# Kernel tuning notes

Measured on AMD Instinct MI355X. Metric: run time of the kernel, lower is better.

The kernel has to match this reference:

```python
import jax, jax.numpy as jnp
import numpy as np

N = 8192      # nodes
K_NN = 32     # kNN neighbors (module default k=32)
E = N * 16    # edges for TAGConv graph
EPS = 1e-5    # BatchNorm eps


def setup_inputs() -> dict:
    key = jax.random.key(0)
    ks = iter(jax.random.split(key, 64))
    def lin(i, o):
        return jax.random.normal(next(ks), (i, o), jnp.float32) / np.float32(np.sqrt(i))
    def vec(c, scale=0.02):
        return jax.random.normal(next(ks), (c,), jnp.float32) * scale
    inp = {}
    inp["pos"] = jax.random.normal(next(ks), (N, 3), jnp.float32)
    inp["x"] = jax.random.normal(next(ks), (N, 4), jnp.float32)
    inp["edge_index"] = jax.random.randint(next(ks), (2, E), 0, N, jnp.int32)
    # conv1 edge-MLP [2*3, 64, 64, 64]
    inp["mlp1_W1"] = lin(6, 64)
    inp["mlp1_W23"] = jnp.stack([lin(64, 64), lin(64, 64)])
    inp["mlp1_b"] = jnp.stack([vec(64) for _ in range(3)])
    inp["mlp1_g"] = 1.0 + jnp.stack([vec(64) for _ in range(3)])
    inp["mlp1_beta"] = jnp.stack([vec(64) for _ in range(3)])
    # conv2 edge-MLP [2*64, 128]
    inp["mlp2_W"] = lin(128, 128); inp["mlp2_b"] = vec(128)
    inp["mlp2_g"] = 1.0 + vec(128); inp["mlp2_beta"] = vec(128)
    # lin1 MLP [128+64, 512]
    inp["lin1_W"] = lin(192, 512); inp["lin1_b"] = vec(512)
    inp["lin1_g"] = 1.0 + vec(512); inp["lin1_beta"] = vec(512)
    # TAGConv(4,64,K=3) and TAGConv(64,128,K=3): K+1 hop weights each, shared bias
    inp["tag1_W"] = jnp.stack([lin(4, 64) for _ in range(4)]); inp["tag1_b"] = vec(64)
    inp["tag2_W"] = jnp.stack([lin(64, 128) for _ in range(4)]); inp["tag2_b"] = vec(128)
    # lin_gcnn1 MLP [128+64, 512]
    inp["lin2_W"] = lin(192, 512); inp["lin2_b"] = vec(512)
    inp["lin2_g"] = 1.0 + vec(512); inp["lin2_beta"] = vec(512)
    # mix_output: MLP[1024,512] -> Dropout -> MLP[512,256] -> Dropout -> Lin(256,1)
    inp["mix1_W"] = lin(1024, 512); inp["mix1_b"] = vec(512)
    inp["mix1_g"] = 1.0 + vec(512); inp["mix1_beta"] = vec(512)
    inp["mix2_W"] = lin(512, 256); inp["mix2_b"] = vec(256)
    inp["mix2_g"] = 1.0 + vec(256); inp["mix2_beta"] = vec(256)
    inp["out_W"] = lin(256, 1); inp["out_b"] = vec(1)
    return inp


def _bn_relu_lin(h, W, b, g, beta):
    # Seq(Linear, ReLU, BatchNorm1d) with training-mode (batch) statistics
    h = jax.nn.relu(h @ W + b)
    mu = jnp.mean(h, axis=0)
    var = jnp.var(h, axis=0)
    return g * (h - mu) * jax.lax.rsqrt(var + EPS) + beta


def _knn_idx(x, k):
    # brute-force kNN (loop=False: self excluded); indices are non-differentiable
    x = jax.lax.stop_gradient(x)
    sq = jnp.sum(x * x, axis=1)
    d = sq[:, None] + sq[None, :] - 2.0 * (x @ x.T)   # [N,N] squared dists
    n = x.shape[0]
    d = d.at[jnp.arange(n), jnp.arange(n)].set(jnp.inf)
    _, idx = jax.lax.top_k(-d, k)
    return idx                                        # [N,k]


def _edge_conv(x, k, mlp_fn):
    # DynamicEdgeConv: kNN graph on x, message MLP([x_i, x_j - x_i]), max-aggregate
    idx = _knn_idx(x, k)
    xj = x[idx]                                       # [N,k,C]
    xi = jnp.broadcast_to(x[:, None, :], xj.shape)
    e = jnp.concatenate([xi, xj - xi], axis=-1).reshape(-1, 2 * x.shape[1])
    h = mlp_fn(e)                                     # [N*k, C_out]
    return jnp.max(h.reshape(x.shape[0], k, -1), axis=1)


def _tag_conv(x, W, b, row, col, norm):
    # TAGConv: out = sum_{m=0..K} (D^-1/2 A D^-1/2)^m x @ W_m + b
    out = x @ W[0]
    h = x
    for m in range(1, W.shape[0]):
        h = jax.ops.segment_sum(norm[:, None] * h[row], col, num_segments=x.shape[0])
        out = out + h @ W[m]
    return out + b


def reference(pos, x, edge_index, mlp1_W1, mlp1_W23, mlp1_b, mlp1_g, mlp1_beta,
              mlp2_W, mlp2_b, mlp2_g, mlp2_beta, lin1_W, lin1_b, lin1_g, lin1_beta,
              tag1_W, tag1_b, tag2_W, tag2_b, lin2_W, lin2_b, lin2_g, lin2_beta,
              mix1_W, mix1_b, mix1_g, mix1_beta, mix2_W, mix2_b, mix2_g, mix2_beta,
              out_W, out_b):
    def mlp1(e):
        h = _bn_relu_lin(e, mlp1_W1, mlp1_b[0], mlp1_g[0], mlp1_beta[0])
        h = _bn_relu_lin(h, mlp1_W23[0], mlp1_b[1], mlp1_g[1], mlp1_beta[1])
        return _bn_relu_lin(h, mlp1_W23[1], mlp1_b[2], mlp1_g[2], mlp1_beta[2])
    def mlp2(e):
        return _bn_relu_lin(e, mlp2_W, mlp2_b, mlp2_g, mlp2_beta)

    # --- DGCNN branch on positions ---
    x1 = _edge_conv(pos, K_NN, mlp1)                  # [N,64]
    x2 = _edge_conv(x1, K_NN, mlp2)                   # [N,128]
    out_dg = _bn_relu_lin(jnp.concatenate([x1, x2], axis=1),
                          lin1_W, lin1_b, lin1_g, lin1_beta)  # [N,512]

    # --- TAGConv branch on node features ---
    row, col = edge_index[0], edge_index[1]
    deg = jax.ops.segment_sum(jnp.ones(row.shape[0], x.dtype), col, num_segments=x.shape[0])
    dinv = jnp.where(deg > 0, jax.lax.rsqrt(jnp.maximum(deg, 1.0)), 0.0)
    norm = dinv[row] * dinv[col]
    g1 = jax.nn.relu(_tag_conv(x, tag1_W, tag1_b, row, col, norm))    # [N,64]
    g2 = jax.nn.relu(_tag_conv(g1, tag2_W, tag2_b, row, col, norm))   # [N,128]
    out_g = _bn_relu_lin(jnp.concatenate([g1, g2], axis=1),
                         lin2_W, lin2_b, lin2_g, lin2_beta)           # [N,512]

    # --- mix head (dropout = identity in eval) ---
    h = jnp.concatenate([out_dg, out_g], axis=1)      # [N,1024]
    h = _bn_relu_lin(h, mix1_W, mix1_b, mix1_g, mix1_beta)
    h = _bn_relu_lin(h, mix2_W, mix2_b, mix2_g, mix2_beta)
    return h @ out_W + out_b                          # [N,1]
```

## Files before the change

kernel.cpp:

```cpp
#include <hip/hip_runtime.h>
#include <cstdint>
#include <cstddef>

#define BN_EPS 1e-5f
#define K1CAP 1024
#define K2CAP 640

typedef short short8 __attribute__((ext_vector_type(8)));
typedef float f32x4 __attribute__((ext_vector_type(4)));
typedef unsigned long long ull;

__device__ __forceinline__ unsigned int ordf(float d) {
  unsigned int u = __float_as_uint(d);
  return (u >> 31) ? ~u : (u | 0x80000000u);
}
__device__ __forceinline__ unsigned short f2bf(float f) {
  unsigned u = __float_as_uint(f);
  u += 0x7fffu + ((u >> 16) & 1u);
  return (unsigned short)(u >> 16);
}
__device__ __forceinline__ float bf2f(unsigned short h) {
  return __uint_as_float(((unsigned)h) << 16);
}

#define BPAD 72

__global__ __launch_bounds__(256)
void mk_gemm_mfma(const float* __restrict__ A,
                  const short* __restrict__ A8h, const short* __restrict__ A8l,
                  const float* __restrict__ src, const int* __restrict__ gidx, int srcC,
                  const float* __restrict__ bnA,
                  const short* __restrict__ Wh, const short* __restrict__ Wl,
                  int ldk, int koff, int lda,
                  const float* __restrict__ bias,
                  float* __restrict__ C, int ldc,
                  int M, int N, int K, int flags,
                  float* __restrict__ statsP,
                  float* __restrict__ mxp, float* __restrict__ mnp) {
  __shared__ short Ah[64][BPAD], Al[64][BPAD], Bh[64][BPAD], Bl[64][BPAD];
  __shared__ float ssum[64], ssq[64];
  int tid = threadIdx.x, lane = tid & 63, wid = tid >> 6;
  int wr = wid >> 1, wc = wid & 1;
  int r0 = blockIdx.x * 64, n0 = blockIdx.y * 64;
  int sr = tid >> 2, sc = (tid & 3) * 16;
  f32x4 zero4 = {0.f, 0.f, 0.f, 0.f};
  f32x4 acc[2][2] = {{zero4, zero4}, {zero4, zero4}};
  short8 rAh[2], rAl[2], rBh[2], rBl[2];

  auto stage = [&](int kt) {
    const short* bh = &Wh[(size_t)(n0 + sr) * ldk + koff + kt + sc];
    const short* bl = &Wl[(size_t)(n0 + sr) * ldk + koff + kt + sc];
    rBh[0] = *(const short8*)bh; rBh[1] = *(const short8*)(bh + 8);
    rBl[0] = *(const short8*)bl; rBl[1] = *(const short8*)(bl + 8);
    if (A8h) {
      const short* ah = &A8h[(size_t)(r0 + sr) * lda + kt + sc];
      const short* al = &A8l[(size_t)(r0 + sr) * lda + kt + sc];
      rAh[0] = *(const short8*)ah; rAh[1] = *(const short8*)(ah + 8);
      rAl[0] = *(const short8*)al; rAl[1] = *(const short8*)(al + 8);
    } else {
      float v[16];
      if (flags & 32) {
        int gr = r0 + sr;
        int i = gr >> 5; int j = gidx[gr];
        const float* pi = &A[(size_t)i * srcC + kt + sc];
        const float* pj = &src[(size_t)j * srcC + kt + sc];
        float va[16], vb[16];
        *(float4*)&va[0]  = *(const float4*)&pi[0];
        *(float4*)&va[4]  = *(const float4*)&pi[4];
        *(float4*)&va[8]  = *(const float4*)&pi[8];
        *(float4*)&va[12] = *(const float4*)&pi[12];
        *(float4*)&vb[0]  = *(const float4*)&pj[0];
        *(float4*)&vb[4]  = *(const float4*)&pj[4];
        *(float4*)&vb[8]  = *(const float4*)&pj[8];
        *(float4*)&vb[12] = *(const float4*)&pj[12];
#pragma unroll
        for (int e = 0; e < 16; ++e) v[e] = fmaxf(va[e] + vb[e], 0.f);
      } else {
        const float* ap = &A[(size_t)(r0 + sr) * lda + kt + sc];
        *(float4*)&v[0]  = *(const float4*)&ap[0];
        *(float4*)&v[4]  = *(const float4*)&ap[4];
        *(float4*)&v[8]  = *(const float4*)&ap[8];
        *(float4*)&v[12] = *(const float4*)&ap[12];
      }
      if (bnA) {
#pragma unroll
        for (int e = 0; e < 16; ++e) {
          int gk = kt + sc + e;
          v[e] = fmaf(bnA[gk], v[e], bnA[1024 + gk]);
        }
      }
#pragma unroll
      for (int e = 0; e < 16; ++e) {
        unsigned short h = f2bf(v[e]);
        rAh[e >> 3][e & 7] = (short)h;
        rAl[e >> 3][e & 7] = (short)f2bf(v[e] - bf2f(h));
      }
    }
  };

  stage(0);
  for (int kt = 0; kt < K; kt += 64) {
    *(short8*)&Ah[sr][sc]     = rAh[0];
    *(short8*)&Ah[sr][sc + 8] = rAh[1];
    *(short8*)&Al[sr][sc]     = rAl[0];
    *(short8*)&Al[sr][sc + 8] = rAl[1];
    *(short8*)&Bh[sr][sc]     = rBh[0];
    *(short8*)&Bh[sr][sc + 8] = rBh[1];
    *(short8*)&Bl[sr][sc]     = rBl[0];
    *(short8*)&Bl[sr][sc + 8] = rBl[1];
    __syncthreads();
    if (kt + 64 < K) stage(kt + 64);
    int ar = wr * 32 + (lane & 15);
    int br = wc * 32 + (lane & 15);
#pragma unroll
    for (int kk = 0; kk < 2; ++kk) {
      int kof = kk * 32 + (lane >> 4) * 8;
      short8 a_h[2], a_l[2], b_h[2], b_l[2];
#pragma unroll
      for (int t = 0; t < 2; ++t) {
        a_h[t] = *(const short8*)&Ah[ar + t * 16][kof];
        a_l[t] = *(const short8*)&Al[ar + t * 16][kof];
        b_h[t] = *(const short8*)&Bh[br + t * 16][kof];
        b_l[t] = *(const short8*)&Bl[br + t * 16][kof];
      }
#pragma unroll
      for (int mt = 0; mt < 2; ++mt)
#pragma unroll
        for (int nt = 0; nt < 2; ++nt) {
          acc[mt][nt] = __builtin_amdgcn_mfma_f32_16x16x32_bf16(a_h[mt], b_h[nt], acc[mt][nt], 0, 0, 0);
          acc[mt][nt] = __builtin_amdgcn_mfma_f32_16x16x32_bf16(a_h[mt], b_l[nt], acc[mt][nt], 0, 0, 0);
          acc[mt][nt] = __builtin_amdgcn_mfma_f32_16x16x32_bf16(a_l[mt], b_h[nt], acc[mt][nt], 0, 0, 0);
        }
    }
    __syncthreads();
  }
  bool dostat = (flags & 8) != 0, domx = (flags & 16) != 0;
  float lsum[2] = {0.f, 0.f}, lsq[2] = {0.f, 0.f};
  float lmx[2] = {-3.4e38f, -3.4e38f}, lmn[2] = {3.4e38f, 3.4e38f};
#pragma unroll
  for (int nt = 0; nt < 2; ++nt) {
    int gc = n0 + wc * 32 + nt * 16 + (lane & 15);
#pragma unroll
    for (int mt = 0; mt < 2; ++mt)
#pragma unroll
      for (int i = 0; i < 4; ++i) {
        int gr = r0 + wr * 32 + mt * 16 + (lane >> 4) * 4 + i;
        float v = acc[mt][nt][i];
        if (bias) v += bias[gc];
        if (flags & 1) v += C[(size_t)gr * ldc + gc];
        if (flags & 2) v = fmaxf(v, 0.f);
        if (!domx) C[(size_t)gr * ldc + gc] = v;
        lsum[nt] += v; lsq[nt] = fmaf(v, v, lsq[nt]);
        lmx[nt] = fmaxf(lmx[nt], v); lmn[nt] = fminf(lmn[nt], v);
      }
  }
  if (dostat || domx) {
#pragma unroll
    for (int nt = 0; nt < 2; ++nt) {
#pragma unroll
      for (int m = 16; m <= 32; m <<= 1) {
        lsum[nt] += __shfl_xor(lsum[nt], m, 64);
        lsq[nt] += __shfl_xor(lsq[nt], m, 64);
        lmx[nt] = fmaxf(lmx[nt], __shfl_xor(lmx[nt], m, 64));
        lmn[nt] = fminf(lmn[nt], __shfl_xor(lmn[nt], m, 64));
      }
    }
    if (domx && lane < 16) {
      int node = blockIdx.x * 2 + wr;
#pragma unroll
      for (int nt = 0; nt < 2; ++nt) {
        int gc = n0 + wc * 32 + nt * 16 + lane;
        mxp[(size_t)node * N + gc] = lmx[nt];
        mnp[(size_t)node * N + gc] = lmn[nt];
      }
    }
    if (dostat) {
      if (tid < 64) { ssum[tid] = 0.f; ssq[tid] = 0.f; }
      __syncthreads();
      if (lane < 16) {
#pragma unroll
        for (int nt = 0; nt < 2; ++nt) {
          int ct = wc * 32 + nt * 16 + lane;
          atomicAdd(&ssum[ct], lsum[nt]);
          atomicAdd(&ssq[ct], lsq[nt]);
        }
      }
      __syncthreads();
      if (tid < 64) {
        int slot = blockIdx.x & 63;
        int gc = n0 + tid;
        atomicAdd(&statsP[(size_t)slot * 1024 + gc], ssum[tid]);
        atomicAdd(&statsP[(size_t)slot * 1024 + 512 + gc], ssq[tid]);
      }
    }
  }
}

__global__ void mk_wcvt(const float* __restrict__ W, short* __restrict__ Wh,
                        short* __restrict__ Wl, int K, int N) {
  int g = blockIdx.x * 256 + threadIdx.x;
  if (g >= K * N) return;
  int k = g / N, n = g - k * N;
  float v = W[g];
  unsigned short h = f2bf(v);
  Wh[(size_t)n * K + k] = (short)h;
  Wl[(size_t)n * K + k] = (short)f2bf(v - bf2f(h));
}
__global__ void mk_wcvt2(const float* __restrict__ W, short* __restrict__ Dh,
                         short* __restrict__ Dl, short* __restrict__ Vh,
                         short* __restrict__ Vl) {
  int g = blockIdx.x * 256 + threadIdx.x;
  if (g >= 64 * 128) return;
  int k = g >> 7, n = g & 127;
  float u = W[k * 128 + n], vv = W[(64 + k) * 128 + n];
  float d = u - vv;
  unsigned short h = f2bf(d);
  Dh[n * 64 + k] = (short)h; Dl[n * 64 + k] = (short)f2bf(d - bf2f(h));
  h = f2bf(vv);
  Vh[n * 64 + k] = (short)h; Vl[n * 64 + k] = (short)f2bf(vv - bf2f(h));
}

__global__ void mk_conv1nodes(const float* __restrict__ pos, const float* __restrict__ W1,
                              const float* __restrict__ b1, float* __restrict__ Pp,
                              float* __restrict__ Qn) {
  int g = blockIdx.x * 256 + threadIdx.x;
  if (g >= 8192 * 64) return;
  int i = g >> 6, c = g & 63;
  float p0 = pos[i * 3], p1 = pos[i * 3 + 1], p2 = pos[i * 3 + 2];
  float q = p0 * W1[192 + c] + p1 * W1[256 + c] + p2 * W1[320 + c];
  Qn[g] = q;
  Pp[g] = p0 * W1[c] + p1 * W1[64 + c] + p2 * W1[128 + c] - q + b1[c];
}

__global__ __launch_bounds__(256)
void mk_stats1(const float* __restrict__ Pp, const float* __restrict__ Qn,
               const int* __restrict__ idx1, float* __restrict__ statsP) {
  __shared__ int sidx[512];
  int tid = threadIdx.x;
  int c = tid & 63, grp = tid >> 6;
  int nb = blockIdx.x * 16;
  if (tid < 256) {
    sidx[tid] = idx1[nb * 32 + tid];
    sidx[tid + 256] = idx1[nb * 32 + 256 + tid];
  }
  __syncthreads();
  float s = 0.f, q = 0.f;
  for (int ln = 0; ln < 16; ++ln) {
    float pv = Pp[(size_t)(nb + ln) * 64 + c];
    for (int e = grp; e < 32; e += 4) {
      int j = sidx[ln * 32 + e];
      float v = fmaxf(pv + Qn[(size_t)j * 64 + c], 0.f);
      s += v; q = fmaf(v, v, q);
    }
  }
  int slot = (blockIdx.x * 4 + grp) & 63;
  atomicAdd(&statsP[(size_t)slot * 1024 + c], s);
  atomicAdd(&statsP[(size_t)slot * 1024 + 512 + c], q);
}

__global__ __launch_bounds__(128)
void mk_econv2(const float* __restrict__ R, const float* __restrict__ T,
               const int* __restrict__ st_i, float* __restrict__ mxp,
               float* __restrict__ mnp, float* __restrict__ statsP) {
  __shared__ int sidx[256];
  int tid = threadIdx.x;
  int nb = blockIdx.x * 8;
  sidx[tid] = st_i[nb * 32 + tid];
  sidx[tid + 128] = st_i[nb * 32 + 128 + tid];
  __syncthreads();
  float s = 0.f, q = 0.f;
  for (int ln = 0; ln < 8; ++ln) {
    int i = nb + ln;
    float rv = R[(size_t)i * 128 + tid];
    float mx = -3.4e38f, mn = 3.4e38f;
    for (int e = 0; e < 32; ++e) {
      int j = sidx[ln * 32 + e];
      float v = fmaxf(rv + T[(size_t)j * 128 + tid], 0.f);
      mx = fmaxf(mx, v); mn = fminf(mn, v);
      s += v; q = fmaf(v, v, q);
    }
    mxp[(size_t)i * 128 + tid] = mx;
    mnp[(size_t)i * 128 + tid] = mn;
  }
  int slot = blockIdx.x & 63;
  atomicAdd(&statsP[(size_t)slot * 1024 + tid], s);
  atomicAdd(&statsP[(size_t)slot * 1024 + 512 + tid], q);
}

__global__ void mk_bnfinS(const float* __restrict__ sb, const float* __restrict__ g,
                          const float* __restrict__ beta, float* __restrict__ bno,
                          float Minv, int Cdim) {
  int c = blockIdx.x * 256 + threadIdx.x;
  if (c >= Cdim) return;
  float s = 0.f, q = 0.f;
  for (int sl = 0; sl < 64; ++sl) {
    s += sb[(size_t)sl * 1024 + c];
    q += sb[(size_t)sl * 1024 + 512 + c];
  }
  float mu = s * Minv;
  float var = q * Minv - mu * mu;
  float a = g[c] * rsqrtf(var + BN_EPS);
  bno[c] = a;
  bno[1024 + c] = beta[c] - a * mu;
}

__global__ void mk_finx1(const float* __restrict__ mx, const float* __restrict__ mn,
                         const float* __restrict__ bn, float* __restrict__ xc,
                         short* __restrict__ x1h, short* __restrict__ x1l) {
  int g = blockIdx.x * 256 + threadIdx.x;
  if (g >= 8192 * 64) return;
  int i = g >> 6, c = g & 63;
  float a = bn[c], b = bn[1024 + c];
  float v = (a > 0.f) ? fmaf(a, mx[g], b) : fmaf(a, mn[g], b);
  xc[(size_t)i * 192 + c] = v;
  unsigned short h = f2bf(v);
  x1h[g] = (short)h;
  x1l[g] = (short)f2bf(v - bf2f(h));
}
__global__ void mk_finx2(const float* __restrict__ mx, const float* __restrict__ mn,
                         const float* __restrict__ bn, float* __restrict__ xcB) {
  int g = blockIdx.x * 256 + threadIdx.x;
  if (g >= 8192 * 128) return;
  int i = g >> 7, c = g & 127;
  float a = bn[c], b = bn[1024 + c];
  xcB[(size_t)i * 192 + c] = (a > 0.f) ? fmaf(a, mx[g], b) : fmaf(a, mn[g], b);
}

__global__ void mk_posq(const float* __restrict__ pos, float4* __restrict__ posq) {
  int i = blockIdx.x * 256 + threadIdx.x;
  if (i >= 8192) return;
  float x = pos[i * 3], y = pos[i * 3 + 1], z = pos[i * 3 + 2];
  float s = fmaf(z, z, fmaf(y, y, x * x));
  posq[i] = make_float4(x, y, z, s);
}

__device__ __forceinline__ unsigned wave_kth8(unsigned v) {
  unsigned T = 0;
#pragma unroll
  for (int b = 31; b >= 0; --b) {
    unsigned cand = T | (1u << b);
    int c = __popcll(__ballot(v < cand));
    if (c < 8) T = cand;
  }
  return T;
}

__global__ __launch_bounds__(256)
void mk_knn1(const float4* __restrict__ posq, int* __restrict__ idxout) {
  __shared__ ull buf[K1CAP];
  __shared__ unsigned Tw[4];
  __shared__ unsigned cnt;
  int q = blockIdx.x, tid = threadIdx.x;
  int lane = tid & 63, wid = tid >> 6;
  float4 pq = posq[q];
  if (tid == 0) cnt = 0;
  unsigned key[32];
  unsigned vmin = 0xFFFFFFFFu;
#pragma unroll
  for (int c = 0; c < 32; ++c) {
    int j = c * 256 + tid;
    float4 pj = posq[j];
    float d = pq.w + pj.w - 2.f * (pq.x * pj.x + pq.y * pj.y + pq.z * pj.z);
    unsigned k = (j == q) ? 0xFFFFFFFFu : ordf(d);
    key[c] = k;
    vmin = vmin < k ? vmin : k;
  }
  unsigned T = wave_kth8(vmin);
  if (lane == 0) Tw[wid] = T;
  __syncthreads();
  unsigned Tmax = max(max(Tw[0], Tw[1]), max(Tw[2], Tw[3]));
#pragma unroll
  for (int c = 0; c < 32; ++c) {
    if (key[c] <= Tmax) {
      int j = c * 256 + tid;
      unsigned s = atomicAdd(&cnt, 1u);
      if (s < K1CAP) buf[s] = (((ull)key[c]) << 32) | (unsigned)j;
    }
  }
  __syncthreads();
  int m = cnt < (unsigned)K1CAP ? (int)cnt : K1CAP;
  for (int e = tid; e < m; e += 256) {
    ull mine = buf[e];
    int rank = 0;
    for (int f = 0; f < m; ++f) rank += (buf[f] < mine) ? 1 : 0;
    if (rank < 32) idxout[q * 32 + rank] = (int)(unsigned)(mine & 0xFFFFFFFFu);
  }
}

__global__ __launch_bounds__(256)
void mk_knn2(const float* __restrict__ S, const float* __restrict__ sq,
             int c0, int first,
             unsigned* __restrict__ st_k, int* __restrict__ st_i) {
  __shared__ ull buf[K2CAP];
  __shared__ unsigned Tw[4];
  __shared__ unsigned cnt;
  int q = blockIdx.x, tid = threadIdx.x;
  int lane = tid & 63, wid = tid >> 6;
  float sqq = sq[q];
  if (tid == 0) cnt = 0;
  unsigned key[8];
  unsigned vmin = 0xFFFFFFFFu;
#pragma unroll
  for (int c = 0; c < 8; ++c) {
    int t = c * 256 + tid;
    int j = c0 + t;
    float d = sqq + sq[j] - 2.f * S[(size_t)q * 2048 + t];
    unsigned k = (j == q) ? 0xFFFFFFFFu : ordf(d);
    key[c] = k;
    vmin = vmin < k ? vmin : k;
  }
  unsigned T = wave_kth8(vmin);
  if (lane == 0) Tw[wid] = T;
  __syncthreads();
  unsigned Tmax = max(max(Tw[0], Tw[1]), max(Tw[2], Tw[3]));
#pragma unroll
  for (int c = 0; c < 8; ++c) {
    if (key[c] <= Tmax) {
      int j = c0 + c * 256 + tid;
      unsigned s = atomicAdd(&cnt, 1u);
      if (s < K2CAP) buf[s] = (((ull)key[c]) << 32) | (unsigned)j;
    }
  }
  if (!first && tid < 32) {
    ull k = (((ull)st_k[q * 32 + tid]) << 32) | (unsigned)st_i[q * 32 + tid];
    unsigned s = atomicAdd(&cnt, 1u);
    if (s < K2CAP) buf[s] = k;
  }
  __syncthreads();
  int m = cnt < (unsigned)K2CAP ? (int)cnt : K2CAP;
  for (int e = tid; e < m; e += 256) {
    ull mine = buf[e];
    int rank = 0;
    for (int f = 0; f < m; ++f) rank += (buf[f] < mine) ? 1 : 0;
    if (rank < 32) {
      st_k[q * 32 + rank] = (unsigned)(mine >> 32);
      st_i[q * 32 + rank] = (int)(unsigned)(mine & 0xFFFFFFFFu);
    }
  }
}

#define GBM 64
#define GBN 64
#define GBK 16

__global__ __launch_bounds__(256)
void mk_gemm(const float* __restrict__ A, const float* __restrict__ W, int ldw,
             const float* __restrict__ bias, float* __restrict__ C, int ldc,
             int M, int N, int K, int flags) {
  __shared__ float As[GBK][GBM + 4];
  __shared__ float Ws[GBK][GBN];
  int tid = threadIdx.x;
  int r0 = blockIdx.x * GBM, n0 = blockIdx.y * GBN;
  int ty = tid >> 4, tx = tid & 15;
  float acc[4][4] = {};
  for (int kt = 0; kt < K; kt += GBK) {
#pragma unroll
    for (int it = 0; it < 4; ++it) {
      int l = it * 256 + tid;
      int r = l >> 4, kk = l & 15;
      int gr = r0 + r, gk = kt + kk;
      float v = 0.f;
      if (gk < K && gr < M) v = A[(size_t)gr * K + gk];
      As[kk][r] = v;
      int kw = l >> 6, nw = l & 63;
      int gkw = kt + kw;
      Ws[kw][nw] = (gkw < K && (n0 + nw) < N) ? W[(size_t)gkw * ldw + n0 + nw] : 0.f;
    }
    __syncthreads();
#pragma unroll
    for (int kk = 0; kk < GBK; ++kk) {
      float4 a4 = *(const float4*)&As[kk][ty * 4];
      float4 b4 = *(const float4*)&Ws[kk][tx * 4];
      float av[4] = {a4.x, a4.y, a4.z, a4.w};
      float bv[4] = {b4.x, b4.y, b4.z, b4.w};
#pragma unroll
      for (int i = 0; i < 4; ++i)
#pragma unroll
        for (int j = 0; j < 4; ++j)
          acc[i][j] = fmaf(av[i], bv[j], acc[i][j]);
    }
    __syncthreads();
  }
#pragma unroll
  for (int i = 0; i < 4; ++i) {
    int gr = r0 + ty * 4 + i;
    if (gr >= M) continue;
#pragma unroll
    for (int j = 0; j < 4; ++j) {
      int gc = n0 + tx * 4 + j;
      if (gc >= N) continue;
      float v = acc[i][j];
      if (bias) v += bias[gc];
      if (flags & 1) v += C[(size_t)gr * ldc + gc];
      if (flags & 2) v = fmaxf(v, 0.f);
      C[(size_t)gr * ldc + gc] = v;
    }
  }
}

__global__ void mk_sqnorm(const float* __restrict__ x, int ld, float* __restrict__ sq,
                          int Npts, int Cdim) {
  int i = blockIdx.x * blockDim.x + threadIdx.x;
  if (i >= Npts) return;
  float s = 0.f;
  for (int c = 0; c < Cdim; ++c) { float v = x[(size_t)i * ld + c]; s = fmaf(v, v, s); }
  sq[i] = s;
}

__global__ void mk_count(const int* __restrict__ col, int* __restrict__ cnt, int E) {
  int e = blockIdx.x * 256 + threadIdx.x;
  if (e < E) atomicAdd(&cnt[col[e]], 1);
}
__global__ __launch_bounds__(1024)
void mk_scan(const int* __restrict__ cnt, int* __restrict__ offp,
             int* __restrict__ cur, float* __restrict__ dinvf) {
  __shared__ int wsum[16];
  __shared__ int wexc[16];
  int t = threadIdx.x, lane = t & 63, w = t >> 6;
  int v[8]; int s = 0;
  int base = t * 8;
#pragma unroll
  for (int k = 0; k < 8; ++k) { v[k] = s; s += cnt[base + k]; }
  int sc = s;
#pragma unroll
  for (int off2 = 1; off2 < 64; off2 <<= 1) {
    int n = __shfl_up(sc, off2, 64);
    if (lane >= off2) sc += n;
  }
  if (lane == 63) wsum[w] = sc;
  __syncthreads();
  if (w == 0) {
    int x = (lane < 16) ? wsum[lane] : 0;
    int scx = x;
#pragma unroll
    for (int off2 = 1; off2 < 16; off2 <<= 1) {
      int n = __shfl_up(scx, off2, 64);
      if (lane >= off2) scx += n;
    }
    if (lane < 16) wexc[lane] = scx - x;
  }
  __syncthreads();
  int texc = wexc[w] + (sc - s);
#pragma unroll
  for (int k = 0; k < 8; ++k) {
    int o = texc + v[k];
    offp[base + k] = o;
    cur[base + k] = o;
    int d = cnt[base + k];
    dinvf[base + k] = (d > 0) ? rsqrtf((float)(d < 1 ? 1 : d)) : 0.f;
  }
  if (t == 1023) offp[8192] = texc + s;
}
__global__ void mk_fill(const int* __restrict__ row, const int* __restrict__ col,
                        const float* __restrict__ dinvf, int* __restrict__ cur,
                        int* __restrict__ crow, float* __restrict__ cw, int E) {
  int e = blockIdx.x * 256 + threadIdx.x;
  if (e >= E) return;
  int c = col[e], r = row[e];
  int s = atomicAdd(&cur[c], 1);
  crow[s] = r;
  cw[s] = dinvf[r] * dinvf[c];
}
__global__ void mk_prop64(const float* __restrict__ in, int in_ld,
                          const int* __restrict__ offp, const int* __restrict__ crow,
                          const float* __restrict__ cw, float* __restrict__ out, int out_ld) {
  int gid = blockIdx.x * 256 + threadIdx.x;
  if (gid >= 8192 * 16) return;
  int col = gid >> 4, c4 = (gid & 15) * 4;
  int s0 = offp[col], s1 = offp[col + 1];
  float a0 = 0, a1 = 0, a2 = 0, a3 = 0;
  for (int s = s0; s < s1; ++s) {
    int r = crow[s]; float w = cw[s];
    float4 v = *(const float4*)&in[(size_t)r * in_ld + c4];
    a0 = fmaf(w, v.x, a0); a1 = fmaf(w, v.y, a1);
    a2 = fmaf(w, v.z, a2); a3 = fmaf(w, v.w, a3);
  }
  float4 o = {a0, a1, a2, a3};
  *(float4*)&out[(size_t)col * out_ld + c4] = o;
}
__global__ void mk_prop4(const float* __restrict__ in, int in_ld,
                         const int* __restrict__ offp, const int* __restrict__ crow,
                         const float* __restrict__ cw, float* __restrict__ out, int out_ld) {
  int col = blockIdx.x * 256 + threadIdx.x;
  if (col >= 8192) return;
  int s0 = offp[col], s1 = offp[col + 1];
  float a0 = 0, a1 = 0, a2 = 0, a3 = 0;
  for (int s = s0; s < s1; ++s) {
    int r = crow[s]; float w = cw[s];
    float4 v = *(const float4*)&in[(size_t)r * in_ld];
    a0 = fmaf(w, v.x, a0); a1 = fmaf(w, v.y, a1);
    a2 = fmaf(w, v.z, a2); a3 = fmaf(w, v.w, a3);
  }
  float4 o = {a0, a1, a2, a3};
  *(float4*)&out[(size_t)col * out_ld] = o;
}
__global__ void mk_pack4(const float* __restrict__ xin, float* __restrict__ H1) {
  int g = blockIdx.x * 256 + threadIdx.x;
  if (g >= 8192 * 4) return;
  H1[(size_t)(g >> 2) * 16 + (g & 3)] = xin[g];
}
__global__ void mk_copy64(const float* __restrict__ gcv, float* __restrict__ H2) {
  int g = blockIdx.x * 256 + threadIdx.x;
  if (g >= 8192 * 64) return;
  H2[(size_t)(g >> 6) * 256 + (g & 63)] = gcv[(size_t)(g >> 6) * 192 + (g & 63)];
}

__global__ __launch_bounds__(256)
void mk_gemv_out(const float* __restrict__ h, const float* __restrict__ bn,
                 const float* __restrict__ w, const float* __restrict__ b,
                 float* __restrict__ out, int Npts) {
  int row = blockIdx.x * 4 + (threadIdx.x >> 6);
  int lane = threadIdx.x & 63;
  if (row >= Npts) return;
  int c = lane * 4;
  float4 v = *(const float4*)&h[(size_t)row * 256 + c];
  float s = (bn[c] * v.x + bn[1024 + c]) * w[c]
          + (bn[c + 1] * v.y + bn[1024 + c + 1]) * w[c + 1]
          + (bn[c + 2] * v.z + bn[1024 + c + 2]) * w[c + 2]
          + (bn[c + 3] * v.w + bn[1024 + c + 3]) * w[c + 3];
#pragma unroll
  for (int off = 32; off; off >>= 1) s += __shfl_xor(s, off, 64);
  if (lane == 0) out[row] = s + b[0];
}

extern "C" void kernel_launch(void* const* d_in, const int* in_sizes, int n_in,
                              void* d_out, int out_size, void* d_ws, size_t ws_size,
                              hipStream_t stream) {
  const int N = 8192;
  const int NE = N * 32;
  const float* pos = (const float*)d_in[0];
  const float* xin = (const float*)d_in[1];
  const int* ei = (const int*)d_in[2];
  const int E = in_sizes[2] / 2;
  const int* erow = ei;
  const int* ecol = ei + E;
  const float* mlp1_W1  = (const float*)d_in[3];
  const float* mlp1_W23 = (const float*)d_in[4];
  const float* mlp1_b   = (const float*)d_in[5];
  const float* mlp1_g   = (const float*)d_in[6];
  const float* mlp1_be  = (const float*)d_in[7];
  const float* mlp2_W   = (const float*)d_in[8];
  const float* mlp2_b   = (const float*)d_in[9];
  const float* mlp2_g   = (const float*)d_in[10];
  const float* mlp2_be  = (const float*)d_in[11];
  const float* lin1_W   = (const float*)d_in[12];
  const float* lin1_b   = (const float*)d_in[13];
  const float* lin1_g   = (const float*)d_in[14];
  const float* lin1_be  = (const float*)d_in[15];
  const float* tag1_W   = (const float*)d_in[16];
  const float* tag1_b   = (const float*)d_in[17];
  const float* tag2_W   = (const float*)d_in[18];
  const float* tag2_b   = (const float*)d_in[19];
  const float* lin2_W   = (const float*)d_in[20];
  const float* lin2_b   = (const float*)d_in[21];
  const float* lin2_g   = (const float*)d_in[22];
  const float* lin2_be  = (const float*)d_in[23];
  const float* mix1_W   = (const float*)d_in[24];
  const float* mix1_b   = (const float*)d_in[25];
  const float* mix1_g   = (const float*)d_in[26];
  const float* mix1_be  = (const float*)d_in[27];
  const float* mix2_W   = (const float*)d_in[28];
  const float* mix2_b   = (const float*)d_in[29];
  const float* mix2_g   = (const float*)d_in[30];
  const float* mix2_be  = (const float*)d_in[31];
  const float* outW     = (const float*)d_in[32];
  const float* outB     = (const float*)d_in[33];

  char* base = (char*)d_ws;
  size_t off = 0;
  auto alloc = [&](size_t b) -> void* {
    void* p = base + off;
    off += (b + 255) & ~(size_t)255;
    return p;
  };
  float* BIG = (float*)alloc(134217728ull);
  float* h2    = BIG;
  float* Sb    = BIG;
  float* mhcat = BIG;
  float* mh1   = BIG + 8388608;
  float* mh2   = BIG + 12582912;
  float* H2    = BIG + 16777216;
  int*   idx1 = (int*)alloc((size_t)NE * 4);
  unsigned* st_k = (unsigned*)alloc((size_t)NE * 4);
  int*   st_i = (int*)alloc((size_t)NE * 4);
  float* xc  = (float*)alloc((size_t)N * 192 * 4);
  float* gc  = (float*)alloc((size_t)N * 192 * 4);
  float4* posq = (float4*)alloc((size_t)N * 16);
  float* sqx = (float*)alloc((size_t)N * 4);
  float* Pp  = (float*)alloc((size_t)N * 64 * 4);
  float* Qn  = (float*)alloc((size_t)N * 64 * 4);
  float* Rb  = (float*)alloc((size_t)N * 128 * 4);
  float* Tb  = (float*)alloc((size_t)N * 128 * 4);
  float* mx1 = (float*)alloc((size_t)N * 64 * 4);
  float* mn1 = (float*)alloc((size_t)N * 64 * 4);
  float* mx2 = (float*)alloc((size_t)N * 128 * 4);
  float* mn2 = (float*)alloc((size_t)N * 128 * 4);
  float* H1  = (float*)alloc((size_t)N * 16 * 4);
  float* dinvf = (float*)alloc((size_t)N * 4);
  int* cnt     = (int*)alloc((size_t)N * 4);
  int* csr_off = (int*)alloc((size_t)(N + 1) * 4);
  int* cursor  = (int*)alloc((size_t)N * 4);
  int* csr_row = (int*)alloc((size_t)E * 4);
  float* csr_w = (float*)alloc((size_t)E * 4);
  float* slotAll = (float*)alloc((size_t)8 * 64 * 1024 * 4);
  auto slot = [&](int i) { return slotAll + (size_t)i * 64 * 1024; };
  float* bnb = (float*)alloc(8 * 2048 * 4);
  auto bnp = [&](int i) { return bnb + (size_t)i * 2048; };
  float* bnM = bnp(4);
  auto salloc = [&](size_t n) { return (short*)alloc(n * 2); };
  short* w23a_h = salloc(4096);   short* w23a_l = salloc(4096);
  short* w23b_h = salloc(4096);   short* w23b_l = salloc(4096);
  short* wd2_h  = salloc(8192);   short* wd2_l  = salloc(8192);
  short* wv2_h  = salloc(8192);   short* wv2_l  = salloc(8192);
  short* wl1_h  = salloc(98304);  short* wl1_l  = salloc(98304);
  short* wt2_h  = salloc(32768);  short* wt2_l  = salloc(32768);
  short* wl2_h  = salloc(98304);  short* wl2_l  = salloc(98304);
  short* wx1_h  = salloc(524288); short* wx1_l  = salloc(524288);
  short* wx2_h  = salloc(131072); short* wx2_l  = salloc(131072);
  short* x1h    = salloc(524288); short* x1l    = salloc(524288);

  auto gemmF = [&](const float* A, const short* A8h, const short* A8l,
                   const float* src, const int* gidx, int srcC, const float* bnA,
                   const short* Wh_, const short* Wl_, int ldk, int koff, int lda,
                   const float* bias, float* Cp, int ldc,
                   int M, int Nn, int Kk, int flags,
                   float* stP = nullptr, float* mxP = nullptr, float* mnP = nullptr) {
    dim3 g(M / 64, Nn / 64);
    mk_gemm_mfma<<<g, 256, 0, stream>>>(A, A8h, A8l, src, gidx, srcC, bnA,
                                        Wh_, Wl_, ldk, koff, lda, bias, Cp, ldc,
                                        M, Nn, Kk, flags, stP, mxP, mnP);
  };
  auto wcvt = [&](const float* W, short* Wh_, short* Wl_, int Kk, int Nn) {
    mk_wcvt<<<(Kk * Nn + 255) / 256, 256, 0, stream>>>(W, Wh_, Wl_, Kk, Nn);
  };

  hipMemsetAsync(slotAll, 0, (size_t)8 * 64 * 1024 * 4, stream);
  hipMemsetAsync(cnt, 0, (size_t)N * 4, stream);
  wcvt(mlp1_W23,        w23a_h, w23a_l, 64, 64);
  wcvt(mlp1_W23 + 4096, w23b_h, w23b_l, 64, 64);
  mk_wcvt2<<<(64 * 128 + 255) / 256, 256, 0, stream>>>(mlp2_W, wd2_h, wd2_l, wv2_h, wv2_l);
  wcvt(lin1_W, wl1_h, wl1_l, 192, 512);
  wcvt(tag2_W, wt2_h, wt2_l, 256, 128);
  wcvt(lin2_W, wl2_h, wl2_l, 192, 512);
  wcvt(mix1_W, wx1_h, wx1_l, 1024, 512);
  wcvt(mix2_W, wx2_h, wx2_l, 512, 256);

  mk_posq<<<32, 256, 0, stream>>>(pos, posq);
  mk_knn1<<<N, 256, 0, stream>>>(posq, idx1);

  mk_conv1nodes<<<(N * 64 + 255) / 256, 256, 0, stream>>>(pos, mlp1_W1, mlp1_b, Pp, Qn);
  mk_stats1<<<512, 256, 0, stream>>>(Pp, Qn, idx1, slot(0));
  mk_bnfinS<<<1, 256, 0, stream>>>(slot(0), mlp1_g, mlp1_be, bnp(0), 1.f / NE, 64);
  gemmF(Pp, nullptr, nullptr, Qn, idx1, 64, bnp(0),
        w23a_h, w23a_l, 64, 0, 64, mlp1_b + 64, h2, 64, NE, 64, 64, 2 | 8 | 32, slot(1));
  mk_bnfinS<<<1, 256, 0, stream>>>(slot(1), mlp1_g + 64, mlp1_be + 64, bnp(1), 1.f / NE, 64);
  gemmF(h2, nullptr, nullptr, nullptr, nullptr, 0, bnp(1),
        w23b_h, w23b_l, 64, 0, 64, mlp1_b + 128, nullptr, 64, NE, 64, 64, 2 | 8 | 16,
        slot(2), mx1, mn1);
  mk_bnfinS<<<1, 256, 0, stream>>>(slot(2), mlp1_g + 128, mlp1_be + 128, bnp(2), 1.f / NE, 64);
  mk_finx1<<<(N * 64 + 255) / 256, 256, 0, stream>>>(mx1, mn1, bnp(2), xc, x1h, x1l);

  mk_sqnorm<<<32, 256, 0, stream>>>(xc, 192, sqx, N, 64);
  for (int c = 0; c < 4; ++c) {
    gemmF(nullptr, x1h, x1l, nullptr, nullptr, 0, nullptr,
          x1h + (size_t)c * 2048 * 64, x1l + (size_t)c * 2048 * 64, 64, 0, 64,
          nullptr, Sb, 2048, N, 2048, 64, 0);
    mk_knn2<<<N, 256, 0, stream>>>(Sb, sqx, c * 2048, c == 0 ? 1 : 0, st_k, st_i);
  }

  gemmF(nullptr, x1h, x1l, nullptr, nullptr, 0, nullptr,
        wd2_h, wd2_l, 64, 0, 64, mlp2_b, Rb, 128, N, 128, 64, 0);
  gemmF(nullptr, x1h, x1l, nullptr, nullptr, 0, nullptr,
        wv2_h, wv2_l, 64, 0, 64, nullptr, Tb, 128, N, 128, 64, 0);
  mk_econv2<<<N / 8, 128, 0, stream>>>(Rb, Tb, st_i, mx2, mn2, slot(3));
  mk_bnfinS<<<1, 256, 0, stream>>>(slot(3), mlp2_g, mlp2_be, bnp(3), 1.f / NE, 128);
  mk_finx2<<<(N * 128 + 255) / 256, 256, 0, stream>>>(mx2, mn2, bnp(3), xc + 64);

  gemmF(xc, nullptr, nullptr, nullptr, nullptr, 0, nullptr,
        wl1_h, wl1_l, 192, 0, 192, lin1_b, mhcat, 1024, N, 512, 192, 2 | 8, slot(4));
  mk_bnfinS<<<2, 256, 0, stream>>>(slot(4), lin1_g, lin1_be, bnM, 1.f / N, 512);

  mk_count<<<(E + 255) / 256, 256, 0, stream>>>(ecol, cnt, E);
  mk_scan<<<1, 1024, 0, stream>>>(cnt, csr_off, cursor, dinvf);
  mk_fill<<<(E + 255) / 256, 256, 0, stream>>>(erow, ecol, dinvf, cursor, csr_row, csr_w, E);
  mk_pack4<<<(N * 4 + 255) / 256, 256, 0, stream>>>(xin, H1);
  mk_prop4<<<32, 256, 0, stream>>>(xin, 4, csr_off, csr_row, csr_w, H1 + 4, 16);
  mk_prop4<<<32, 256, 0, stream>>>(H1 + 4, 16, csr_off, csr_row, csr_w, H1 + 8, 16);
  mk_prop4<<<32, 256, 0, stream>>>(H1 + 8, 16, csr_off, csr_row, csr_w, H1 + 12, 16);
  mk_gemm<<<dim3(128, 1), 256, 0, stream>>>(H1, tag1_W, 64, tag1_b, gc, 192, N, 64, 16, 2);
  mk_copy64<<<(N * 64 + 255) / 256, 256, 0, stream>>>(gc, H2);
  mk_prop64<<<512, 256, 0, stream>>>(gc, 192, csr_off, csr_row, csr_w, H2 + 64, 256);
  mk_prop64<<<512, 256, 0, stream>>>(H2 + 64, 256, csr_off, csr_row, csr_w, H2 + 128, 256);
  mk_prop64<<<512, 256, 0, stream>>>(H2 + 128, 256, csr_off, csr_row, csr_w, H2 + 192, 256);
  gemmF(H2, nullptr, nullptr, nullptr, nullptr, 0, nullptr,
        wt2_h, wt2_l, 256, 0, 256, tag2_b, gc + 64, 192, N, 128, 256, 2);
  gemmF(gc, nullptr, nullptr, nullptr, nullptr, 0, nullptr,
        wl2_h, wl2_l, 192, 0, 192, lin2_b, mhcat + 512, 1024, N, 512, 192, 2 | 8, slot(5));
  mk_bnfinS<<<2, 256, 0, stream>>>(slot(5), lin2_g, lin2_be, bnM + 512, 1.f / N, 512);

  gemmF(mhcat, nullptr, nullptr, nullptr, nullptr, 0, bnM,
        wx1_h, wx1_l, 1024, 0, 1024, mix1_b, mh1, 512, N, 512, 1024, 2 | 8, slot(6));
  mk_bnfinS<<<2, 256, 0, stream>>>(slot(6), mix1_g, mix1_be, bnp(6), 1.f / N, 512);
  gemmF(mh1, nullptr, nullptr, nullptr, nullptr, 0, bnp(6),
        wx2_h, wx2_l, 512, 0, 512, mix2_b, mh2, 256, N, 256, 512, 2 | 8, slot(7));
  mk_bnfinS<<<1, 256, 0, stream>>>(slot(7), mix2_g, mix2_be, bnp(7), 1.f / N, 256);
  mk_gemv_out<<<N / 4, 256, 0, stream>>>(mh2, bnp(7), outW, outB, (float*)d_out, N);
}
```

Before: 737.8 us.

## Fold BatchNorm affine into mix-head weights and store bf16 hi/lo activations

The BatchNorm scale and shift that used to be applied to the mix-head GEMM inputs are now folded into the weights: the scale multiplies the weights during bf16 hi/lo conversion, and the shift is pushed through the weights into a new bias. The lin1, lin2 and mix1 GEMMs now write their outputs directly as bf16 hi/lo pairs, so the next GEMM reads pre-split A operands instead of converting fp32 and applying BN per tile. This removes per-element BN and split work from the large K=1024 and K=512 GEMMs and shrinks activation traffic. In exchange it adds small weight-conversion and bias-fold kernels per call and changes the rounding order slightly.

```diff
diff --git a/kernel.cpp b/kernel.cpp
--- a/kernel.cpp
+++ b/kernel.cpp
@@ -33,7 +33,8 @@
                   const short* __restrict__ Wh, const short* __restrict__ Wl,
                   int ldk, int koff, int lda,
                   const float* __restrict__ bias,
-                  float* __restrict__ C, int ldc,
+                  float* __restrict__ C, short* __restrict__ Ch, short* __restrict__ Cl,
+                  int ldc,
                   int M, int N, int K, int flags,
                   float* __restrict__ statsP,
                   float* __restrict__ mxp, float* __restrict__ mnp) {
@@ -149,7 +150,15 @@
         if (bias) v += bias[gc];
         if (flags & 1) v += C[(size_t)gr * ldc + gc];
         if (flags & 2) v = fmaxf(v, 0.f);
-        if (!domx) C[(size_t)gr * ldc + gc] = v;
+        if (!domx) {
+          if (flags & 64) {
+            unsigned short hh = f2bf(v);
+            Ch[(size_t)gr * ldc + gc] = (short)hh;
+            Cl[(size_t)gr * ldc + gc] = (short)f2bf(v - bf2f(hh));
+          } else {
+            C[(size_t)gr * ldc + gc] = v;
+          }
+        }
         lsum[nt] += v; lsq[nt] = fmaf(v, v, lsq[nt]);
         lmx[nt] = fmaxf(lmx[nt], v); lmn[nt] = fminf(lmn[nt], v);
       }
@@ -205,6 +214,28 @@
   unsigned short h = f2bf(v);
   Wh[(size_t)n * K + k] = (short)h;
   Wl[(size_t)n * K + k] = (short)f2bf(v - bf2f(h));
+}
+__global__ void mk_wcvts(const float* __restrict__ W, const float* __restrict__ a,
+                         short* __restrict__ Wh, short* __restrict__ Wl, int K, int N) {
+  int g = blockIdx.x * 256 + threadIdx.x;
+  if (g >= K * N) return;
+  int k = g / N, n = g - k * N;
+  float v = a[k] * W[g];
+  unsigned short h = f2bf(v);
+  Wh[(size_t)n * K + k] = (short)h;
+  Wl[(size_t)n * K + k] = (short)f2bf(v - bf2f(h));
+}
+__global__ void mk_biasfold(const float* __restrict__ W, const float* __restrict__ bv,
+                            const float* __restrict__ b0, float* __restrict__ bo,
+                            int K, int N) {
+  int col = blockIdx.x * 4 + (threadIdx.x >> 6);
+  int lane = threadIdx.x & 63;
+  if (col >= N) return;
+  float s = 0.f;
+  for (int k = lane; k < K; k += 64) s = fmaf(bv[k], W[(size_t)k * N + col], s);
+#pragma unroll
+  for (int off = 32; off; off >>= 1) s += __shfl_xor(s, off, 64);
+  if (lane == 0) bo[col] = b0[col] + s;
 }
 __global__ void mk_wcvt2(const float* __restrict__ W, short* __restrict__ Dh,
                          short* __restrict__ Dl, short* __restrict__ Vh,
@@ -676,10 +707,12 @@
   float* BIG = (float*)alloc(134217728ull);
   float* h2    = BIG;
   float* Sb    = BIG;
-  float* mhcat = BIG;
-  float* mh1   = BIG + 8388608;
-  float* mh2   = BIG + 12582912;
-  float* H2    = BIG + 16777216;
+  short* mhcat_h = (short*)BIG;
+  short* mhcat_l = (short*)((char*)BIG + 16777216);
+  short* mh1_h   = (short*)((char*)BIG + 33554432);
+  short* mh1_l   = (short*)((char*)BIG + 41943040);
+  float* mh2     = (float*)((char*)BIG + 50331648);
+  float* H2      = BIG + 16777216;
   int*   idx1 = (int*)alloc((size_t)NE * 4);
   unsigned* st_k = (unsigned*)alloc((size_t)NE * 4);
   int*   st_i = (int*)alloc((size_t)NE * 4);
@@ -707,6 +740,8 @@
   float* bnb = (float*)alloc(8 * 2048 * 4);
   auto bnp = [&](int i) { return bnb + (size_t)i * 2048; };
   float* bnM = bnp(4);
+  float* bias1f = (float*)alloc(512 * 4);
+  float* bias2f = (float*)alloc(256 * 4);
   auto salloc = [&](size_t n) { return (short*)alloc(n * 2); };
   short* w23a_h = salloc(4096);   short* w23a_l = salloc(4096);
   short* w23b_h = salloc(4096);   short* w23b_l = salloc(4096);
@@ -722,12 +757,12 @@
   auto gemmF = [&](const float* A, const short* A8h, const short* A8l,
                    const float* src, const int* gidx, int srcC, const float* bnA,
                    const short* Wh_, const short* Wl_, int ldk, int koff, int lda,
-                   const float* bias, float* Cp, int ldc,
+                   const float* bias, float* Cp, short* Chp, short* Clp, int ldc,
                    int M, int Nn, int Kk, int flags,
                    float* stP = nullptr, float* mxP = nullptr, float* mnP = nullptr) {
     dim3 g(M / 64, Nn / 64);
     mk_gemm_mfma<<<g, 256, 0, stream>>>(A, A8h, A8l, src, gidx, srcC, bnA,
-                                        Wh_, Wl_, ldk, koff, lda, bias, Cp, ldc,
+                                        Wh_, Wl_, ldk, koff, lda, bias, Cp, Chp, Clp, ldc,
                                         M, Nn, Kk, flags, stP, mxP, mnP);
   };
   auto wcvt = [&](const float* W, short* Wh_, short* Wl_, int Kk, int Nn) {
@@ -742,8 +777,6 @@
   wcvt(lin1_W, wl1_h, wl1_l, 192, 512);
   wcvt(tag2_W, wt2_h, wt2_l, 256, 128);
   wcvt(lin2_W, wl2_h, wl2_l, 192, 512);
-  wcvt(mix1_W, wx1_h, wx1_l, 1024, 512);
-  wcvt(mix2_W, wx2_h, wx2_l, 512, 256);
 
   mk_posq<<<32, 256, 0, stream>>>(pos, posq);
   mk_knn1<<<N, 256, 0, stream>>>(posq, idx1);
@@ -752,11 +785,12 @@
   mk_stats1<<<512, 256, 0, stream>>>(Pp, Qn, idx1, slot(0));
   mk_bnfinS<<<1, 256, 0, stream>>>(slot(0), mlp1_g, mlp1_be, bnp(0), 1.f / NE, 64);
   gemmF(Pp, nullptr, nullptr, Qn, idx1, 64, bnp(0),
-        w23a_h, w23a_l, 64, 0, 64, mlp1_b + 64, h2, 64, NE, 64, 64, 2 | 8 | 32, slot(1));
+        w23a_h, w23a_l, 64, 0, 64, mlp1_b + 64, h2, nullptr, nullptr, 64,
+        NE, 64, 64, 2 | 8 | 32, slot(1));
   mk_bnfinS<<<1, 256, 0, stream>>>(slot(1), mlp1_g + 64, mlp1_be + 64, bnp(1), 1.f / NE, 64);
   gemmF(h2, nullptr, nullptr, nullptr, nullptr, 0, bnp(1),
-        w23b_h, w23b_l, 64, 0, 64, mlp1_b + 128, nullptr, 64, NE, 64, 64, 2 | 8 | 16,
-        slot(2), mx1, mn1);
+        w23b_h, w23b_l, 64, 0, 64, mlp1_b + 128, nullptr, nullptr, nullptr, 64,
+        NE, 64, 64, 2 | 8 | 16, slot(2), mx1, mn1);
   mk_bnfinS<<<1, 256, 0, stream>>>(slot(2), mlp1_g + 128, mlp1_be + 128, bnp(2), 1.f / NE, 64);
   mk_finx1<<<(N * 64 + 255) / 256, 256, 0, stream>>>(mx1, mn1, bnp(2), xc, x1h, x1l);
 
@@ -764,20 +798,21 @@
   for (int c = 0; c < 4; ++c) {
     gemmF(nullptr, x1h, x1l, nullptr, nullptr, 0, nullptr,
           x1h + (size_t)c * 2048 * 64, x1l + (size_t)c * 2048 * 64, 64, 0, 64,
-          nullptr, Sb, 2048, N, 2048, 64, 0);
+          nullptr, Sb, nullptr, nullptr, 2048, N, 2048, 64, 0);
     mk_knn2<<<N, 256, 0, stream>>>(Sb, sqx, c * 2048, c == 0 ? 1 : 0, st_k, st_i);
   }
 
   gemmF(nullptr, x1h, x1l, nullptr, nullptr, 0, nullptr,
-        wd2_h, wd2_l, 64, 0, 64, mlp2_b, Rb, 128, N, 128, 64, 0);
+        wd2_h, wd2_l, 64, 0, 64, mlp2_b, Rb, nullptr, nullptr, 128, N, 128, 64, 0);
   gemmF(nullptr, x1h, x1l, nullptr, nullptr, 0, nullptr,
-        wv2_h, wv2_l, 64, 0, 64, nullptr, Tb, 128, N, 128, 64, 0);
+        wv2_h, wv2_l, 64, 0, 64, nullptr, Tb, nullptr, nullptr, 128, N, 128, 64, 0);
   mk_econv2<<<N / 8, 128, 0, stream>>>(Rb, Tb, st_i, mx2, mn2, slot(3));
   mk_bnfinS<<<1, 256, 0, stream>>>(slot(3), mlp2_g, mlp2_be, bnp(3), 1.f / NE, 128);
   mk_finx2<<<(N * 128 + 255) / 256, 256, 0, stream>>>(mx2, mn2, bnp(3), xc + 64);
 
   gemmF(xc, nullptr, nullptr, nullptr, nullptr, 0, nullptr,
-        wl1_h, wl1_l, 192, 0, 192, lin1_b, mhcat, 1024, N, 512, 192, 2 | 8, slot(4));
+        wl1_h, wl1_l, 192, 0, 192, lin1_b, nullptr, mhcat_h, mhcat_l, 1024,
+        N, 512, 192, 2 | 8 | 64, slot(4));
   mk_bnfinS<<<2, 256, 0, stream>>>(slot(4), lin1_g, lin1_be, bnM, 1.f / N, 512);
 
   mk_count<<<(E + 255) / 256, 256, 0, stream>>>(ecol, cnt, E);
@@ -793,16 +828,24 @@
   mk_prop64<<<512, 256, 0, stream>>>(H2 + 64, 256, csr_off, csr_row, csr_w, H2 + 128, 256);
   mk_prop64<<<512, 256, 0, stream>>>(H2 + 128, 256, csr_off, csr_row, csr_w, H2 + 192, 256);
   gemmF(H2, nullptr, nullptr, nullptr, nullptr, 0, nullptr,
-        wt2_h, wt2_l, 256, 0, 256, tag2_b, gc + 64, 192, N, 128, 256, 2);
+        wt2_h, wt2_l, 256, 0, 256, tag2_b, gc + 64, nullptr, nullptr, 192,
+        N, 128, 256, 2);
   gemmF(gc, nullptr, nullptr, nullptr, nullptr, 0, nullptr,
-        wl2_h, wl2_l, 192, 0, 192, lin2_b, mhcat + 512, 1024, N, 512, 192, 2 | 8, slot(5));
+        wl2_h, wl2_l, 192, 0, 192, lin2_b, nullptr, mhcat_h + 512, mhcat_l + 512, 1024,
+        N, 512, 192, 2 | 8 | 64, slot(5));
   mk_bnfinS<<<2, 256, 0, stream>>>(slot(5), lin2_g, lin2_be, bnM + 512, 1.f / N, 512);
 
-  gemmF(mhcat, nullptr, nullptr, nullptr, nullptr, 0, bnM,
-        wx1_h, wx1_l, 1024, 0, 1024, mix1_b, mh1, 512, N, 512, 1024, 2 | 8, slot(6));
+  mk_wcvts<<<(1024 * 512 + 255) / 256, 256, 0, stream>>>(mix1_W, bnM, wx1_h, wx1_l, 1024, 512);
+  mk_biasfold<<<128, 256, 0, stream>>>(mix1_W, bnM + 1024, mix1_b, bias1f, 1024, 512);
+  gemmF(nullptr, mhcat_h, mhcat_l, nullptr, nullptr, 0, nullptr,
+        wx1_h, wx1_l, 1024, 0, 1024, bias1f, nullptr, mh1_h, mh1_l, 512,
+        N, 512, 1024, 2 | 8 | 64, slot(6));
   mk_bnfinS<<<2, 256, 0, stream>>>(slot(6), mix1_g, mix1_be, bnp(6), 1.f / N, 512);
-  gemmF(mh1, nullptr, nullptr, nullptr, nullptr, 0, bnp(6),
-        wx2_h, wx2_l, 512, 0, 512, mix2_b, mh2, 256, N, 256, 512, 2 | 8, slot(7));
+  mk_wcvts<<<(512 * 256 + 255) / 256, 256, 0, stream>>>(mix2_W, bnp(6), wx2_h, wx2_l, 512, 256);
+  mk_biasfold<<<64, 256, 0, stream>>>(mix2_W, bnp(6) + 1024, mix2_b, bias2f, 512, 256);
+  gemmF(nullptr, mh1_h, mh1_l, nullptr, nullptr, 0, nullptr,
+        wx2_h, wx2_l, 512, 0, 512, bias2f, mh2, nullptr, nullptr, 256,
+        N, 256, 512, 2 | 8, slot(7));
   mk_bnfinS<<<1, 256, 0, stream>>>(slot(7), mix2_g, mix2_be, bnp(7), 1.f / N, 256);
   mk_gemv_out<<<N / 4, 256, 0, stream>>>(mh2, bnp(7), outW, outB, (float*)d_out, N);
 }
```

After: 718.4 us. 2.6% less time.
